# Kernel tuning notes

Measured on AMD Instinct MI355X. Metric: run time of the kernel, lower is better.

## Reference

```python
import jax, jax.numpy as jnp
import numpy as np

H = 512

def setup_inputs() -> dict:
    key = jax.random.key(0)
    ks = jax.random.split(key, 24)
    B, Tv, Tt = 64, 512, 64
    def W(k):
        return jax.random.normal(k, (H, H), dtype=jnp.float32) * 0.01
    def v(k):
        return jax.random.normal(k, (H,), dtype=jnp.float32) * 0.01
    return {
        "h": jax.random.normal(ks[0], (B, H), dtype=jnp.float32),
        "hidden_frames": jax.random.normal(ks[1], (B, Tv, H), dtype=jnp.float32),
        "hidden_text": jax.random.normal(ks[2], (B, Tt, H), dtype=jnp.float32),
        "Wav": W(ks[3]), "Wat": W(ks[4]), "Uav": W(ks[5]), "Uat": W(ks[6]),
        "Vav": v(ks[7]), "Vat": v(ks[8]),
        "bav": jnp.zeros((H,), jnp.float32), "bat": jnp.zeros((H,), jnp.float32),
        "Whh": W(ks[9]), "bh": jnp.zeros((H,), jnp.float32),
        "Wve": jax.random.normal(ks[10], (H, H), dtype=jnp.float32) * 0.02,
        "bve": jnp.zeros((H,), jnp.float32),
        "Wqe": jax.random.normal(ks[11], (H, H), dtype=jnp.float32) * 0.02,
        "bqe": jnp.zeros((H,), jnp.float32),
        "Wb": W(ks[12]), "Vbv": W(ks[13]), "Vbt": W(ks[14]),
        "bbv": jnp.zeros((H,), jnp.float32), "bbt": jnp.zeros((H,), jnp.float32),
        "wb": v(ks[15]),
    }

def reference(h, hidden_frames, hidden_text, Wav, Wat, Uav, Uat, Vav, Vat,
              bav, bat, Whh, bh, Wve, bve, Wqe, bqe, Wb, Vbv, Vbt, bbv, bbt, wb):
    # Additive (Bahdanau) attention over frames, conditioned on h
    Uhv = (h @ Uav)[:, None, :]                                   # [B,1,H]
    Uht = (h @ Uat)[:, None, :]
    score_v = jnp.tanh(hidden_frames @ Wav + Uhv + bav) @ Vav     # [B,Tv]
    score_t = jnp.tanh(hidden_text @ Wat + Uht + bat) @ Vat       # [B,Tt]
    av = jax.nn.softmax(score_v, axis=1)
    at = jax.nn.softmax(score_t, axis=1)
    hv_sum = jnp.einsum('bt,bth->bh', av, hidden_frames)          # [B,H]
    ht_sum = jnp.einsum('bt,bth->bh', at, hidden_text)
    hv_sum2 = hv_sum @ Wve.T + bve                                # Linear encoders
    ht_sum2 = ht_sum @ Wqe.T + bqe
    # Gating between the two streams (blp is None -> concat path)
    Wbs = h @ Wb
    mt1 = ht_sum @ Vbt + bbt + Wbs
    mv1 = hv_sum @ Vbv + bbv + Wbs
    mtv = jnp.tanh(jnp.concatenate([mv1, mt1], axis=0))           # [2B,H]
    beta = jax.nn.softmax(mtv @ wb, axis=0)                       # [2B]
    out = jnp.tanh(h @ Whh + beta[0] * hv_sum2 + beta[1] * ht_sum2 + bh)
    return out                                                     # [B,H]
```

## Files before the change

### kernel.cpp

```cpp
#include <hip/hip_runtime.h>
#include <stdint.h>
#include <stddef.h>

#define H  512
#define BB 64
#define TV 512
#define TT 64

typedef short s8v __attribute__((ext_vector_type(8)));
typedef float f4v __attribute__((ext_vector_type(4)));


__device__ inline unsigned short f2bf(float f) {
  unsigned int u = __float_as_uint(f);
  u = (u + 0x7fffu + ((u >> 16) & 1u)) >> 16;
  return (unsigned short)u;
}

__device__ inline unsigned int pk2bf(float lo, float hi) {
  unsigned int a = __float_as_uint(lo);
  a = (a + 0x7fffu + ((a >> 16) & 1u)) >> 16;
  unsigned int b = __float_as_uint(hi);
  b = (b + 0x7fffu + ((b >> 16) & 1u)) & 0xffff0000u;
  return a | b;
}

__device__ inline float fast_tanh(float x) {
  x = fminf(15.f, fmaxf(-15.f, x));
  float e = __expf(2.f * x);
  return (e - 1.f) * __builtin_amdgcn_rcpf(e + 1.f);
}

__device__ inline void gld16(const unsigned short* g, unsigned short* l) {
  __builtin_amdgcn_global_load_lds(
      (const __attribute__((address_space(1))) unsigned int*)g,
      (__attribute__((address_space(3))) unsigned int*)l, 16, 0, 0);
}

__global__ void k_prep(const float* __restrict__ F, const float* __restrict__ Txt,
                       const float* __restrict__ h,
                       const float* __restrict__ Wav, const float* __restrict__ Wat,
                       const float* __restrict__ Uav, const float* __restrict__ Uat,
                       const float* __restrict__ Wb,  const float* __restrict__ Whh,
                       const float* __restrict__ Wve, const float* __restrict__ Wqe,
                       const float* __restrict__ Vbv, const float* __restrict__ Vbt,
                       unsigned short* __restrict__ Fb, unsigned short* __restrict__ Tb,
                       unsigned short* __restrict__ hb, unsigned short* __restrict__ Wbf) {
  __shared__ float tile[64][65];
  const int bx = blockIdx.x, tid = threadIdx.x;
  if (bx < 9232) {
    const float* src; unsigned short* dst; size_t base;
    if (bx < 8192)      { base = (size_t)bx * 2048;          src = F;   dst = Fb; }
    else if (bx < 9216) { base = (size_t)(bx - 8192) * 2048; src = Txt; dst = Tb; }
    else                { base = (size_t)(bx - 9216) * 2048; src = h;   dst = hb; }
    size_t i = base + (size_t)tid * 8;
    float4 f0 = *(const float4*)(src + i);
    float4 f1 = *(const float4*)(src + i + 4);
    uint4 p;
    p.x = pk2bf(f0.x, f0.y); p.y = pk2bf(f0.z, f0.w);
    p.z = pk2bf(f1.x, f1.y); p.w = pk2bf(f1.z, f1.w);
    *(uint4*)(dst + i) = p;
    return;
  }
  const int z = (bx - 9232) >> 6;
  const int t = (bx - 9232) & 63;
  const int k0 = (t >> 3) * 64, j0 = (t & 7) * 64;
  const float* src =
      (z == 0) ? Wav : (z == 1) ? Wat : (z == 2) ? Uav : (z == 3) ? Uat :
      (z == 4) ? Wb  : (z == 5) ? Whh : (z == 6) ? Wve : (z == 7) ? Wqe :
      (z == 8) ? Vbv : Vbt;
  unsigned short* dst = Wbf + (size_t)z * H * H;
  if (z == 6 || z == 7) {
    for (int i = 0; i < 16; ++i) {
      int e = tid + i * 256; int r = e >> 6, c = e & 63;
      dst[(size_t)(k0 + r) * H + j0 + c] = f2bf(src[(size_t)(k0 + r) * H + j0 + c]);
    }
    return;
  }
  for (int i = 0; i < 16; ++i) {
    int e = tid + i * 256; int r = e >> 6, c = e & 63;
    tile[r][c] = src[(size_t)(k0 + r) * H + j0 + c];
  }
  __syncthreads();
  for (int i = 0; i < 16; ++i) {
    int e = tid + i * 256; int r = e >> 6, c = e & 63;
    dst[(size_t)(j0 + r) * H + k0 + c] = f2bf(tile[c][r]);
  }
}

__global__ __launch_bounds__(256)
void k_gemmA(const unsigned short* __restrict__ A0, const unsigned short* __restrict__ Bt,
             float* __restrict__ C,
             const float* __restrict__ bias0, const float* __restrict__ bias1) {
  __shared__ unsigned short As[64 * 32];
  __shared__ unsigned short Bs[64 * 32];
  const int tid = threadIdx.x;
  const int n0 = blockIdx.x * 64;
  const int seg = blockIdx.y;
  const unsigned short* B = Bt + (size_t)seg * H * H;

  const int r = tid >> 2, c = (tid & 3) * 8;
  const unsigned short* Ag = A0 + (size_t)r * H + c;
  const unsigned short* Bg = B + (size_t)(n0 + r) * H + c;
  unsigned short* Al = &As[tid * 8];
  unsigned short* Bl = &Bs[tid * 8];

  const int wv = tid >> 6, ln = tid & 63;
  const int quad = ln >> 4, l16 = ln & 15;
  const int wm = (wv >> 1) * 32, wn = (wv & 1) * 32;

  f4v acc[2][2] = {};
  for (int k0 = 0; k0 < H; k0 += 32) {
    __syncthreads();
    gld16(Ag + k0, Al);
    gld16(Bg + k0, Bl);
    __syncthreads();
    s8v afr[2], bfr[2];
#pragma unroll
    for (int mi = 0; mi < 2; ++mi)
      afr[mi] = *(const s8v*)&As[(wm + mi * 16 + l16) * 32 + quad * 8];
#pragma unroll
    for (int ni = 0; ni < 2; ++ni)
      bfr[ni] = *(const s8v*)&Bs[(wn + ni * 16 + l16) * 32 + quad * 8];
#pragma unroll
    for (int mi = 0; mi < 2; ++mi)
#pragma unroll
      for (int ni = 0; ni < 2; ++ni)
        acc[mi][ni] = __builtin_amdgcn_mfma_f32_16x16x32_bf16(afr[mi], bfr[ni], acc[mi][ni], 0, 0, 0);
  }

  const float* bias = (seg == 0) ? bias0 : (seg == 1) ? bias1 : nullptr;
  float* Cs = C + (size_t)seg * BB * H;
#pragma unroll
  for (int mi = 0; mi < 2; ++mi)
#pragma unroll
    for (int ni = 0; ni < 2; ++ni)
#pragma unroll
      for (int rr = 0; rr < 4; ++rr) {
        const int row = wm + mi * 16 + quad * 4 + rr;
        const int j = n0 + wn + ni * 16 + l16;
        float v = acc[mi][ni][rr];
        if (bias) v += bias[j];
        Cs[(size_t)row * H + j] = v;
      }
}

__global__ __launch_bounds__(256)
void k_score(const unsigned short* __restrict__ Fb, const unsigned short* __restrict__ Tb,
             const unsigned short* __restrict__ Wbf,
             const float* __restrict__ uv, const float* __restrict__ ut,
             const float* __restrict__ Vav, const float* __restrict__ Vat,
             float* __restrict__ score_v, float* __restrict__ score_t) {
  __shared__ unsigned short As[128 * 32];
  __shared__ unsigned short Bs[128 * 32];
  const int tid = threadIdx.x;
  const int bx = blockIdx.x;
  const bool fr = bx < 256;
  const int m0 = (fr ? bx : bx - 256) * 128;
  const int n0 = blockIdx.y * 128;
  const int logT = fr ? 9 : 6;
  const unsigned short* A = fr ? Fb : Tb;
  const unsigned short* Bt = fr ? Wbf : (Wbf + (size_t)H * H);
  const float* uvw = fr ? uv : ut;
  const float* V = fr ? Vav : Vat;
  float* score = fr ? score_v : score_t;

  const int wv = tid >> 6, ln = tid & 63;
  const int quad = ln >> 4, l16 = ln & 15;
  const int wm = (wv >> 1) * 64, wn = (wv & 1) * 64;

  const int s0 = wv * 128 + ln;
  const int s1 = s0 + 64;
  const int r0 = s0 >> 2, c0 = (s0 & 3) * 8;
  const int r1 = s1 >> 2, c1 = (s1 & 3) * 8;

  const unsigned short* Ag0 = A + (size_t)(m0 + r0) * H + c0;
  const unsigned short* Ag1 = A + (size_t)(m0 + r1) * H + c1;
  const unsigned short* Bg0 = Bt + (size_t)(n0 + r0) * H + c0;
  const unsigned short* Bg1 = Bt + (size_t)(n0 + r1) * H + c1;
  unsigned short* Al0 = &As[s0 * 8];
  unsigned short* Al1 = &As[s1 * 8];
  unsigned short* Bl0 = &Bs[s0 * 8];
  unsigned short* Bl1 = &Bs[s1 * 8];

  f4v acc[4][4] = {};

  for (int k0 = 0; k0 < H; k0 += 32) {
    __syncthreads();
    gld16(Ag0 + k0, Al0);
    gld16(Ag1 + k0, Al1);
    gld16(Bg0 + k0, Bl0);
    gld16(Bg1 + k0, Bl1);
    __syncthreads();
    s8v afr[4], bfr[4];
#pragma unroll
    for (int mi = 0; mi < 4; ++mi)
      afr[mi] = *(const s8v*)&As[(wm + mi * 16 + l16) * 32 + quad * 8];
#pragma unroll
    for (int ni = 0; ni < 4; ++ni)
      bfr[ni] = *(const s8v*)&Bs[(wn + ni * 16 + l16) * 32 + quad * 8];
#pragma unroll
    for (int mi = 0; mi < 4; ++mi)
#pragma unroll
      for (int ni = 0; ni < 4; ++ni)
        acc[mi][ni] = __builtin_amdgcn_mfma_f32_16x16x32_bf16(afr[mi], bfr[ni], acc[mi][ni], 0, 0, 0);
  }

  int jj[4]; float vv[4];
#pragma unroll
  for (int ni = 0; ni < 4; ++ni) {
    jj[ni] = n0 + wn + ni * 16 + l16;
    vv[ni] = V[jj[ni]];
  }
  const int tmask = (1 << logT) - 1;
#pragma unroll
  for (int mi = 0; mi < 4; ++mi) {
    const int mrow0 = m0 + wm + mi * 16;
    const int bidx = mrow0 >> logT;
    const float* up = uvw + (size_t)bidx * H;
    float uu[4];
#pragma unroll
    for (int ni = 0; ni < 4; ++ni) uu[ni] = up[jj[ni]];
#pragma unroll
    for (int r = 0; r < 4; ++r) {
      float sum = 0.f;
#pragma unroll
      for (int ni = 0; ni < 4; ++ni)
        sum += fast_tanh(acc[mi][ni][r] + uu[ni]) * vv[ni];
      sum += __shfl_xor(sum, 1);
      sum += __shfl_xor(sum, 2);
      sum += __shfl_xor(sum, 4);
      sum += __shfl_xor(sum, 8);
      if (l16 == 0) {
        const int mrow = mrow0 + quad * 4 + r;
        atomicAdd(&score[((size_t)bidx << logT) + (mrow & tmask)], sum);
      }
    }
  }
}

__global__ void k_wsum(const unsigned short* __restrict__ Fb, const unsigned short* __restrict__ Tb,
                       const float* __restrict__ score_v, const float* __restrict__ score_t,
                       float* __restrict__ hv_sum, float* __restrict__ ht_sum) {
  __shared__ float w[64];
  __shared__ float red[4];
  const int b = blockIdx.x, ch = blockIdx.y, tid = threadIdx.x;
  const bool fr = ch < 8;
  const float* sc = fr ? (score_v + b * TV) : (score_t + b * TT);
  const int T = fr ? TV : TT;

  float v0 = (tid < T) ? sc[tid] : -1e30f;
  float v1 = fr ? sc[tid + 256] : -1e30f;
  float mx = fmaxf(v0, v1);
  for (int d = 32; d; d >>= 1) mx = fmaxf(mx, __shfl_xor(mx, d));
  if ((tid & 63) == 0) red[tid >> 6] = mx;
  __syncthreads();
  mx = fmaxf(fmaxf(red[0], red[1]), fmaxf(red[2], red[3]));
  __syncthreads();
  float e0 = (tid < T) ? __expf(v0 - mx) : 0.f;
  float e1 = fr ? __expf(v1 - mx) : 0.f;
  float se = e0 + e1;
  for (int d = 32; d; d >>= 1) se += __shfl_xor(se, d);
  if ((tid & 63) == 0) red[tid >> 6] = se;
  __syncthreads();
  const float inv = 1.f / (red[0] + red[1] + red[2] + red[3]);
  const int t0 = fr ? ch * 64 : 0;
  if (tid < 64) w[tid] = __expf(sc[t0 + tid] - mx) * inv;
  __syncthreads();

  const unsigned short* X = fr ? (Fb + ((size_t)b * TV + t0) * H)
                               : (Tb + (size_t)b * TT * H);
  float* out = fr ? (hv_sum + b * H) : (ht_sum + b * H);
  const int j = tid * 2;
  float a0 = 0.f, a1 = 0.f;
  for (int t = 0; t < 64; ++t) {
    unsigned u = *(const unsigned*)(X + (size_t)t * H + j);
    float wt = w[t];
    a0 += wt * __uint_as_float(u << 16);
    a1 += wt * __uint_as_float(u & 0xffff0000u);
  }
  atomicAdd(&out[j], a0);
  atomicAdd(&out[j + 1], a1);
}

__global__ __launch_bounds__(256)
void k_gemmB(const float* __restrict__ Afp, const unsigned short* __restrict__ Bt,
             float* __restrict__ C, const float* __restrict__ wbs,
             const float* __restrict__ bbv, const float* __restrict__ bbt,
             const float* __restrict__ wb, float* __restrict__ sArr) {
  __shared__ unsigned short As[64 * 32];
  __shared__ unsigned short Bs[64 * 32];
  const int tid = threadIdx.x;
  const int n0 = blockIdx.x * 64;
  const int seg = blockIdx.y;
  const float* A = Afp + (size_t)((seg & 1) ? BB * H : 0);
  const unsigned short* B = Bt + (size_t)seg * H * H;

  const int r = tid >> 2, c = (tid & 3) * 8;
  const float* Ag = A + (size_t)r * H + c;
  const unsigned short* Bg = B + (size_t)(n0 + r) * H + c;
  unsigned short* Bl = &Bs[tid * 8];

  const int wv = tid >> 6, ln = tid & 63;
  const int quad = ln >> 4, l16 = ln & 15;
  const int wm = (wv >> 1) * 32, wn = (wv & 1) * 32;

  f4v acc[2][2] = {};
  for (int k0 = 0; k0 < H; k0 += 32) {
    __syncthreads();
    float4 f0 = *(const float4*)(Ag + k0);
    float4 f1 = *(const float4*)(Ag + k0 + 4);
    uint4 p;
    p.x = pk2bf(f0.x, f0.y); p.y = pk2bf(f0.z, f0.w);
    p.z = pk2bf(f1.x, f1.y); p.w = pk2bf(f1.z, f1.w);
    *(uint4*)&As[tid * 8] = p;
    gld16(Bg + k0, Bl);
    __syncthreads();
    s8v afr[2], bfr[2];
#pragma unroll
    for (int mi = 0; mi < 2; ++mi)
      afr[mi] = *(const s8v*)&As[(wm + mi * 16 + l16) * 32 + quad * 8];
#pragma unroll
    for (int ni = 0; ni < 2; ++ni)
      bfr[ni] = *(const s8v*)&Bs[(wn + ni * 16 + l16) * 32 + quad * 8];
#pragma unroll
    for (int mi = 0; mi < 2; ++mi)
#pragma unroll
      for (int ni = 0; ni < 2; ++ni)
        acc[mi][ni] = __builtin_amdgcn_mfma_f32_16x16x32_bf16(afr[mi], bfr[ni], acc[mi][ni], 0, 0, 0);
  }

  if (seg < 2) {
    float* Cs = C + (size_t)seg * BB * H;
#pragma unroll
    for (int mi = 0; mi < 2; ++mi)
#pragma unroll
      for (int ni = 0; ni < 2; ++ni)
#pragma unroll
        for (int rr = 0; rr < 4; ++rr) {
          const int row = wm + mi * 16 + quad * 4 + rr;
          const int j = n0 + wn + ni * 16 + l16;
          Cs[(size_t)row * H + j] = acc[mi][ni][rr];
        }
  } else {
    const float* b2 = (seg == 2) ? bbv : bbt;
    const int sbase = (seg == 2) ? 0 : BB;
#pragma unroll
    for (int mi = 0; mi < 2; ++mi)
#pragma unroll
      for (int rr = 0; rr < 4; ++rr) {
        const int row = wm + mi * 16 + quad * 4 + rr;
        float sum = 0.f;
#pragma unroll
        for (int ni = 0; ni < 2; ++ni) {
          const int j = n0 + wn + ni * 16 + l16;
          float g = acc[mi][ni][rr] + wbs[(size_t)row * H + j] + b2[j];
          sum += fast_tanh(g) * wb[j];
        }
        sum += __shfl_xor(sum, 1);
        sum += __shfl_xor(sum, 2);
        sum += __shfl_xor(sum, 4);
        sum += __shfl_xor(sum, 8);
        if (l16 == 0) atomicAdd(&sArr[sbase + row], sum);
      }
  }
}

__global__ void k_final2(const float* __restrict__ sArr, const float* __restrict__ hwhh,
                         const float* __restrict__ bh,
                         const float* __restrict__ hv2, const float* __restrict__ ht2,
                         const float* __restrict__ bve, const float* __restrict__ bqe,
                         float* __restrict__ out) {
  __shared__ float red[4];
  const int b = blockIdx.x, tid = threadIdx.x;
  float v = (tid < 2 * BB) ? sArr[tid] : -1e30f;
  float mx = v;
  for (int d = 32; d; d >>= 1) mx = fmaxf(mx, __shfl_xor(mx, d));
  if ((tid & 63) == 0) red[tid >> 6] = mx;
  __syncthreads();
  mx = fmaxf(fmaxf(red[0], red[1]), fmaxf(red[2], red[3]));
  __syncthreads();
  float e = (tid < 2 * BB) ? __expf(v - mx) : 0.f;
  for (int d = 32; d; d >>= 1) e += __shfl_xor(e, d);
  if ((tid & 63) == 0) red[tid >> 6] = e;
  __syncthreads();
  const float Z = red[0] + red[1] + red[2] + red[3];
  const float beta0 = __expf(sArr[0] - mx) / Z;
  const float beta1 = __expf(sArr[1] - mx) / Z;
#pragma unroll
  for (int jj = 0; jj < 2; ++jj) {
    int j = tid + jj * 256;
    float x = hwhh[(size_t)b * H + j] + bh[j]
            + beta0 * (hv2[(size_t)b * H + j] + bve[j])
            + beta1 * (ht2[(size_t)b * H + j] + bqe[j]);
    out[(size_t)b * H + j] = fast_tanh(x);
  }
}


extern "C" void kernel_launch(void* const* d_in, const int* in_sizes, int n_in,
                              void* d_out, int out_size, void* d_ws, size_t ws_size,
                              hipStream_t stream) {
  const float* h    = (const float*)d_in[0];
  const float* F    = (const float*)d_in[1];
  const float* Txt  = (const float*)d_in[2];
  const float* Wav  = (const float*)d_in[3];
  const float* Wat  = (const float*)d_in[4];
  const float* Uav  = (const float*)d_in[5];
  const float* Uat  = (const float*)d_in[6];
  const float* Vav  = (const float*)d_in[7];
  const float* Vat  = (const float*)d_in[8];
  const float* bav  = (const float*)d_in[9];
  const float* bat  = (const float*)d_in[10];
  const float* Whh  = (const float*)d_in[11];
  const float* bh   = (const float*)d_in[12];
  const float* Wve  = (const float*)d_in[13];
  const float* bve  = (const float*)d_in[14];
  const float* Wqe  = (const float*)d_in[15];
  const float* bqe  = (const float*)d_in[16];
  const float* Wb   = (const float*)d_in[17];
  const float* Vbv  = (const float*)d_in[18];
  const float* Vbt  = (const float*)d_in[19];
  const float* bbv  = (const float*)d_in[20];
  const float* bbt  = (const float*)d_in[21];
  const float* wb   = (const float*)d_in[22];
  float* out = (float*)d_out;

  char* ws = (char*)d_ws;
  size_t off = 0;
  auto alloc = [&](size_t bytes) -> void* {
    void* p = ws + off;
    off += (bytes + 255) & ~(size_t)255;
    return p;
  };
  float* score_v = (float*)alloc((size_t)BB * TV * 4);
  float* score_t = (float*)alloc((size_t)BB * TT * 4);
  float* hv_sum  = (float*)alloc((size_t)BB * H * 4);
  float* ht_sum  = (float*)alloc((size_t)BB * H * 4);
  float* sArr    = (float*)alloc((size_t)2 * BB * 4);
  unsigned short* Wbf = (unsigned short*)alloc((size_t)10 * H * H * 2);
  unsigned short* Fb  = (unsigned short*)alloc((size_t)BB * TV * H * 2);
  unsigned short* Tb  = (unsigned short*)alloc((size_t)BB * TT * H * 2);
  unsigned short* hb  = (unsigned short*)alloc((size_t)BB * H * 2);
  float* CA   = (float*)alloc((size_t)4 * BB * H * 4);
  float* CB   = (float*)alloc((size_t)2 * BB * H * 4);

  float* uv   = CA;
  float* ut   = CA + (size_t)BB * H;
  float* wbs  = CA + (size_t)2 * BB * H;
  float* hwhh = CA + (size_t)3 * BB * H;

  hipMemsetAsync(score_v, 0,
                 (size_t)(BB * TV + BB * TT + 2 * BB * H + 2 * BB) * 4, stream);

  k_prep<<<dim3(9872), 256, 0, stream>>>(F, Txt, h, Wav, Wat, Uav, Uat, Wb, Whh,
                                         Wve, Wqe, Vbv, Vbt, Fb, Tb, hb, Wbf);
  k_gemmA<<<dim3(8, 4), 256, 0, stream>>>(hb, Wbf + (size_t)2 * H * H, CA, bav, bat);
  k_score<<<dim3(288, 4), 256, 0, stream>>>(Fb, Tb, Wbf, uv, ut, Vav, Vat,
                                            score_v, score_t);
  k_wsum<<<dim3(64, 9), 256, 0, stream>>>(Fb, Tb, score_v, score_t, hv_sum, ht_sum);
  k_gemmB<<<dim3(8, 4), 256, 0, stream>>>(hv_sum, Wbf + (size_t)6 * H * H, CB,
                                          wbs, bbv, bbt, wb, sArr);
  k_final2<<<64, 256, 0, stream>>>(sArr, hwhh, bh, CB, CB + (size_t)BB * H,
                                   bve, bqe, out);
}
```

Baseline: 227.7 us.

## Restructure score GEMM into single-wave blocks with 128x64 tiles, no barriers

The k_score kernel goes from 256-thread blocks, where four waves share a 128x128 LDS tile, to 64-thread single-wave blocks. Each wave now computes a 128x64 tile on its own, so the launch grid doubles along N. With only one wave per block, the __syncthreads barriers around each K step are dropped and the loads are issued straight into private LDS. The cost is that the frames/text A tiles are now fetched by eight N-blocks instead of four, which doubles A global traffic. It also relies on in-wave ordering of LDS writes and reads being correct without barriers.

Result: slower. 278.2 us (+22.2%).

```diff
diff --git a/kernel.cpp b/kernel.cpp
--- a/kernel.cpp
+++ b/kernel.cpp
@@ -145,19 +145,19 @@
       }
 }
 
-__global__ __launch_bounds__(256)
+__global__ __launch_bounds__(64)
 void k_score(const unsigned short* __restrict__ Fb, const unsigned short* __restrict__ Tb,
              const unsigned short* __restrict__ Wbf,
              const float* __restrict__ uv, const float* __restrict__ ut,
              const float* __restrict__ Vav, const float* __restrict__ Vat,
              float* __restrict__ score_v, float* __restrict__ score_t) {
   __shared__ unsigned short As[128 * 32];
-  __shared__ unsigned short Bs[128 * 32];
-  const int tid = threadIdx.x;
+  __shared__ unsigned short Bs[64 * 32];
+  const int ln = threadIdx.x;
   const int bx = blockIdx.x;
   const bool fr = bx < 256;
   const int m0 = (fr ? bx : bx - 256) * 128;
-  const int n0 = blockIdx.y * 128;
+  const int n0 = blockIdx.y * 64;
   const int logT = fr ? 9 : 6;
   const unsigned short* A = fr ? Fb : Tb;
   const unsigned short* Bt = fr ? Wbf : (Wbf + (size_t)H * H);
@@ -165,57 +165,46 @@
   const float* V = fr ? Vav : Vat;
   float* score = fr ? score_v : score_t;
 
-  const int wv = tid >> 6, ln = tid & 63;
   const int quad = ln >> 4, l16 = ln & 15;
-  const int wm = (wv >> 1) * 64, wn = (wv & 1) * 64;
-
-  const int s0 = wv * 128 + ln;
-  const int s1 = s0 + 64;
-  const int r0 = s0 >> 2, c0 = (s0 & 3) * 8;
-  const int r1 = s1 >> 2, c1 = (s1 & 3) * 8;
-
-  const unsigned short* Ag0 = A + (size_t)(m0 + r0) * H + c0;
-  const unsigned short* Ag1 = A + (size_t)(m0 + r1) * H + c1;
-  const unsigned short* Bg0 = Bt + (size_t)(n0 + r0) * H + c0;
-  const unsigned short* Bg1 = Bt + (size_t)(n0 + r1) * H + c1;
-  unsigned short* Al0 = &As[s0 * 8];
-  unsigned short* Al1 = &As[s1 * 8];
-  unsigned short* Bl0 = &Bs[s0 * 8];
-  unsigned short* Bl1 = &Bs[s1 * 8];
-
-  f4v acc[4][4] = {};
+
+  const int ar = ln >> 2, ac = (ln & 3) * 8;
+  const unsigned short* Ag = A + (size_t)(m0 + ar) * H + ac;
+  const unsigned short* Bg = Bt + (size_t)(n0 + ar) * H + ac;
+  unsigned short* Al = &As[ln * 8];
+  unsigned short* Bl = &Bs[ln * 8];
+
+  f4v acc[8][4] = {};
 
   for (int k0 = 0; k0 < H; k0 += 32) {
-    __syncthreads();
-    gld16(Ag0 + k0, Al0);
-    gld16(Ag1 + k0, Al1);
-    gld16(Bg0 + k0, Bl0);
-    gld16(Bg1 + k0, Bl1);
-    __syncthreads();
-    s8v afr[4], bfr[4];
-#pragma unroll
-    for (int mi = 0; mi < 4; ++mi)
-      afr[mi] = *(const s8v*)&As[(wm + mi * 16 + l16) * 32 + quad * 8];
+#pragma unroll
+    for (int i = 0; i < 8; ++i)
+      gld16(Ag + (size_t)(i * 16) * H + k0, Al + i * 512);
+#pragma unroll
+    for (int i = 0; i < 4; ++i)
+      gld16(Bg + (size_t)(i * 16) * H + k0, Bl + i * 512);
+    s8v bfr[4];
 #pragma unroll
     for (int ni = 0; ni < 4; ++ni)
-      bfr[ni] = *(const s8v*)&Bs[(wn + ni * 16 + l16) * 32 + quad * 8];
-#pragma unroll
-    for (int mi = 0; mi < 4; ++mi)
+      bfr[ni] = *(const s8v*)&Bs[(ni * 16 + l16) * 32 + quad * 8];
+#pragma unroll
+    for (int mi = 0; mi < 8; ++mi) {
+      s8v afr = *(const s8v*)&As[(mi * 16 + l16) * 32 + quad * 8];
 #pragma unroll
       for (int ni = 0; ni < 4; ++ni)
-        acc[mi][ni] = __builtin_amdgcn_mfma_f32_16x16x32_bf16(afr[mi], bfr[ni], acc[mi][ni], 0, 0, 0);
+        acc[mi][ni] = __builtin_amdgcn_mfma_f32_16x16x32_bf16(afr, bfr[ni], acc[mi][ni], 0, 0, 0);
+    }
   }
 
   int jj[4]; float vv[4];
 #pragma unroll
   for (int ni = 0; ni < 4; ++ni) {
-    jj[ni] = n0 + wn + ni * 16 + l16;
+    jj[ni] = n0 + ni * 16 + l16;
     vv[ni] = V[jj[ni]];
   }
   const int tmask = (1 << logT) - 1;
 #pragma unroll
-  for (int mi = 0; mi < 4; ++mi) {
-    const int mrow0 = m0 + wm + mi * 16;
+  for (int mi = 0; mi < 8; ++mi) {
+    const int mrow0 = m0 + mi * 16;
     const int bidx = mrow0 >> logT;
     const float* up = uvw + (size_t)bidx * H;
     float uu[4];
@@ -456,8 +445,8 @@
   k_prep<<<dim3(9872), 256, 0, stream>>>(F, Txt, h, Wav, Wat, Uav, Uat, Wb, Whh,
                                          Wve, Wqe, Vbv, Vbt, Fb, Tb, hb, Wbf);
   k_gemmA<<<dim3(8, 4), 256, 0, stream>>>(hb, Wbf + (size_t)2 * H * H, CA, bav, bat);
-  k_score<<<dim3(288, 4), 256, 0, stream>>>(Fb, Tb, Wbf, uv, ut, Vav, Vat,
-                                            score_v, score_t);
+  k_score<<<dim3(288, 8), 64, 0, stream>>>(Fb, Tb, Wbf, uv, ut, Vav, Vat,
+                                           score_v, score_t);
   k_wsum<<<dim3(64, 9), 256, 0, stream>>>(Fb, Tb, score_v, score_t, hv_sum, ht_sum);
   k_gemmB<<<dim3(8, 4), 256, 0, stream>>>(hv_sum, Wbf + (size_t)6 * H * H, CB,
                                           wbs, bbv, bbt, wb, sArr);
```
